# Performance work log

Measured on AMD Instinct MI355X. Metric: run time of the kernel, lower is better.

Reference implementation:

```python
import jax, jax.numpy as jnp
import numpy as np

T, B, V, D, H = 64, 256, 50000, 300, 512


def setup_inputs() -> dict:
    key = jax.random.key(0)
    ks = jax.random.split(key, 12)
    return {
        "s1": jax.random.randint(ks[0], (T, B), 0, V, dtype=jnp.int32),
        "s2": jax.random.randint(ks[1], (T, B), 0, V, dtype=jnp.int32),
        "emb_table": jax.random.normal(ks[2], (V, D), dtype=jnp.float32),
        "W_ih": jax.random.normal(ks[3], (4 * H, D), dtype=jnp.float32) * 0.2 / np.sqrt(H * D),
        "W_hh": jax.random.normal(ks[4], (4 * H, H), dtype=jnp.float32) * 0.2 / np.sqrt(H),
        "b_ih": jax.random.uniform(ks[5], (4 * H,), dtype=jnp.float32, minval=-0.5, maxval=0.5).at[H:2 * H].set(2.5),
        "b_hh": jax.random.uniform(ks[6], (4 * H,), dtype=jnp.float32, minval=-0.5, maxval=0.5).at[H:2 * H].set(2.5),
        "h0_a": 0.2 * jax.random.normal(ks[7], (B, H), dtype=jnp.float32),
        "c0_a": 0.2 * jax.random.normal(ks[8], (B, H), dtype=jnp.float32),
        "h0_b": 0.2 * jax.random.normal(ks[9], (B, H), dtype=jnp.float32),
        "c0_b": 0.2 * jax.random.normal(ks[10], (B, H), dtype=jnp.float32),
        "is_singleton": 0,
    }


def _lstm_final_hidden(xs, h0, c0, W_ih, W_hh, b_ih, b_hh):
    # xs: [T, B, D]; PyTorch gate order i, f, g, o. Returns final hidden [B, H].
    # Precompute input projections for all timesteps in one GEMM.
    x_proj = jnp.einsum("tbd,gd->tbg", xs, W_ih) + b_ih + b_hh  # [T, B, 4H]

    def step(carry, xp):
        h, c = carry
        gates = xp + h @ W_hh.T  # [B, 4H]
        i, f, g, o = jnp.split(gates, 4, axis=-1)
        c = jax.nn.sigmoid(f) * c + jax.nn.sigmoid(i) * jnp.tanh(g)
        h = jax.nn.sigmoid(o) * jnp.tanh(c)
        return (h, c), None

    (h, c), _ = jax.lax.scan(step, (h0, c0), x_proj)
    return h


def reference(s1, s2, emb_table, W_ih, W_hh, b_ih, b_hh, h0_a, c0_a, h0_b, c0_b, is_singleton):
    xa = emb_table[s1]  # [T, B, D]
    xb = emb_table[s2]
    ha = _lstm_final_hidden(xa, h0_a, c0_a, W_ih, W_hh, b_ih, b_hh)  # [B, H]
    hb = _lstm_final_hidden(xb, h0_b, c0_b, W_ih, W_hh, b_ih, b_hh)
    diff = jnp.abs(ha - hb)
    if is_singleton:
        return jnp.exp(-jnp.sum(diff))  # scalar
    return jnp.exp(-jnp.sum(diff, axis=1))  # [B]
```

## Files before the change

### kernel.cpp

```cpp
#include <hip/hip_runtime.h>
#include <hip/hip_bf16.h>
#include <math.h>

#define TT 64
#define BB 256
#define BT 512
#define DD 300
#define HH 512
#define G4 2048
#define KX 320
#define KW 512
#define KC 64
#define NCHX 5
#define NCHH 8

typedef __attribute__((ext_vector_type(8))) short short8v;
typedef __attribute__((ext_vector_type(4))) float f32x4;
typedef __attribute__((ext_vector_type(4))) unsigned short ushort4v;

__device__ __forceinline__ unsigned short f2bf(float f) {
    union { float f; unsigned int u; } v; v.f = f;
    unsigned int u = v.u;
    u += 0x7fffu + ((u >> 16) & 1u);
    return (unsigned short)(u >> 16);
}
__device__ __forceinline__ float bf2f(unsigned short s) {
    union { unsigned int u; float f; } v; v.u = ((unsigned int)s) << 16;
    return v.f;
}
__device__ __forceinline__ float sigm(float x) { return 1.0f / (1.0f + __expf(-x)); }
__device__ __forceinline__ float tanh_f(float x) {
    float ax = fabsf(x);
    if (ax > 15.0f) return (x > 0.0f) ? 1.0f : -1.0f;
    float e = __expf(2.0f * ax);
    float t = 1.0f - 2.0f / (e + 1.0f);
    return (x >= 0.0f) ? t : -t;
}

__global__ __launch_bounds__(256) void prep_w(const float* __restrict__ Wih,
                                              const float* __restrict__ Whh,
                                              const float* __restrict__ bih,
                                              const float* __restrict__ bhh,
                                              unsigned short* __restrict__ WcatP,
                                              unsigned short* __restrict__ WihP,
                                              float* __restrict__ biasP)
{
    const int gp = blockIdx.x;
    const int jt = gp >> 6, r = gp & 63;
    const int grp = r >> 4, jj = r & 15;
    const int g = grp * 512 + jt * 16 + jj;

    for (int k = threadIdx.x; k < KW; k += 256)
        WcatP[(size_t)gp * KW + k] = f2bf(Whh[(size_t)g * HH + k]);
    for (int k = threadIdx.x; k < KX; k += 256)
        WihP[(size_t)gp * KX + k] = (k < DD) ? f2bf(Wih[(size_t)g * DD + k])
                                             : (unsigned short)0;
    if (threadIdx.x == 0) biasP[jt * 64 + jj * 4 + grp] = bih[g] + bhh[g];
}

__global__ __launch_bounds__(256) void prep_h(const float* __restrict__ h0a,
                                              const float* __restrict__ c0a,
                                              const float* __restrict__ h0b,
                                              const float* __restrict__ c0b,
                                              unsigned short* __restrict__ hhi,
                                              unsigned short* __restrict__ hlo,
                                              float* __restrict__ c)
{
    const int b = blockIdx.x;
    for (int j = threadIdx.x; j < HH; j += 256) {
        float hv = (b < BB) ? h0a[b * HH + j] : h0b[(b - BB) * HH + j];
        float cv = (b < BB) ? c0a[b * HH + j] : c0b[(b - BB) * HH + j];
        unsigned short hi = f2bf(hv);
        hhi[b * HH + j] = hi;
        hlo[b * HH + j] = f2bf(hv - bf2f(hi));
        c[b * HH + j] = cv;
    }
}

__global__ __launch_bounds__(256) void gather_x(const int* __restrict__ s1,
                                                const int* __restrict__ s2,
                                                const float* __restrict__ emb,
                                                unsigned short* __restrict__ Xbf)
{
    const int idx = blockIdx.x * 256 + threadIdx.x;
    const int row = idx / 40;
    const int seg = idx - row * 40;
    const int t = row >> 9;
    const int b = row & 511;
    const int tok = (b < BB) ? s1[t * BB + b] : s2[t * BB + (b - BB)];
    const int k = seg * 8;
    short8v v;
    if (k + 8 <= DD) {
        const float* e0 = emb + (size_t)tok * DD + k;
        float4 va = *(const float4*)e0;
        float4 vb = *(const float4*)(e0 + 4);
        v[0] = (short)f2bf(va.x); v[1] = (short)f2bf(va.y);
        v[2] = (short)f2bf(va.z); v[3] = (short)f2bf(va.w);
        v[4] = (short)f2bf(vb.x); v[5] = (short)f2bf(vb.y);
        v[6] = (short)f2bf(vb.z); v[7] = (short)f2bf(vb.w);
    } else {
        #pragma unroll
        for (int e = 0; e < 8; ++e) {
            int c = k + e;
            v[e] = (c < DD) ? (short)f2bf(emb[(size_t)tok * DD + c]) : (short)0;
        }
    }
    *(short8v*)&Xbf[(size_t)row * KX + k] = v;
}

__global__ __launch_bounds__(512) void gemm_x(
    const unsigned short* __restrict__ Xbf,
    const unsigned short* __restrict__ WihP,
    unsigned short* __restrict__ xprojP)
{
    __shared__ __align__(16) unsigned short smem[16896];
    unsigned short* const As = smem;
    unsigned short* const Bs = smem + 8192;

    const int tid = threadIdx.x;
    const int xcd   = blockIdx.x & 7;
    const int local = blockIdx.x >> 3;
    const int mblk  = xcd * 32 + (local >> 4);
    const int nblk  = local & 15;

    const int lane = tid & 63;
    const int wv  = tid >> 6;
    const int wr2 = wv >> 2;
    const int wc4 = wv & 3;
    const int r16 = lane & 15;
    const int kg8 = lane >> 4;

    const int srow = tid >> 2;
    const int q2   = (tid & 3) * 2;

    f32x4 acc[4][2] = {};

    auto load_chunk = [&](int ch, short8v* va, short8v* vb) {
        const int k0 = ch * KC;
        #pragma unroll
        for (int e = 0; e < 2; ++e) {
            va[e] = *(const short8v*)(Xbf + (size_t)(mblk * 128 + srow) * KX + k0 + (q2 + e) * 8);
            vb[e] = *(const short8v*)(WihP + (size_t)(nblk * 128 + srow) * KX + k0 + (q2 + e) * 8);
        }
    };
    auto write_chunk = [&](const short8v* va, const short8v* vb) {
        #pragma unroll
        for (int e = 0; e < 2; ++e) {
            const int g = ((q2 + e) ^ (srow & 7)) << 3;
            *(short8v*)&As[srow * 64 + g] = va[e];
            *(short8v*)&Bs[srow * 64 + g] = vb[e];
        }
    };
    auto lidx = [&](int r, int ko) { return r * 64 + ((((ko) >> 3) ^ (r & 7)) << 3); };

    short8v va[2], vb[2], na[2], nb[2];
    load_chunk(0, va, vb);
    for (int ch = 0; ch < NCHX; ++ch) {
        write_chunk(va, vb);
        if (ch + 1 < NCHX) load_chunk(ch + 1, na, nb);
        __syncthreads();
        #pragma unroll
        for (int ks = 0; ks < KC; ks += 32) {
            const int ko = ks + kg8 * 8;
            short8v a[4], b[2];
            #pragma unroll
            for (int i = 0; i < 4; ++i)
                a[i] = *(const short8v*)&As[lidx(64 * wr2 + 16 * i + r16, ko)];
            #pragma unroll
            for (int j = 0; j < 2; ++j)
                b[j] = *(const short8v*)&Bs[lidx(32 * wc4 + 16 * j + r16, ko)];
            #pragma unroll
            for (int i = 0; i < 4; ++i)
                #pragma unroll
                for (int j = 0; j < 2; ++j)
                    acc[i][j] = __builtin_amdgcn_mfma_f32_16x16x32_bf16(a[i], b[j], acc[i][j], 0, 0, 0);
        }
        __syncthreads();
        #pragma unroll
        for (int e = 0; e < 2; ++e) { va[e] = na[e]; vb[e] = nb[e]; }
    }

    float* gbuf = (float*)smem;
    const int jj5 = tid & 31;
    const int hh  = jj5 >> 4;
    const int jj  = jj5 & 15;
    const int row0 = tid >> 5;
    #pragma unroll
    for (int p = 0; p < 2; ++p) {
        if (p) __syncthreads();
        if (wr2 == p) {
            #pragma unroll
            for (int i = 0; i < 4; ++i)
                #pragma unroll
                for (int j = 0; j < 2; ++j)
                    #pragma unroll
                    for (int r = 0; r < 4; ++r)
                        gbuf[(16 * i + 4 * kg8 + r) * 132 + 32 * wc4 + 16 * j + r16]
                            = acc[i][j][r];
        }
        __syncthreads();
        #pragma unroll
        for (int u = 0; u < 4; ++u) {
            const int row = row0 + 16 * u;
            const size_t m = (size_t)(mblk * 128 + p * 64 + row);
            ushort4v o;
            #pragma unroll
            for (int grp = 0; grp < 4; ++grp)
                o[grp] = f2bf(gbuf[row * 132 + hh * 64 + grp * 16 + jj]);
            __builtin_nontemporal_store(o,
                (ushort4v*)&xprojP[m * G4 + (nblk * 2 + hh) * 64 + jj * 4]);
        }
    }
}

__global__ __launch_bounds__(256) void lstm_step(
    const unsigned short* __restrict__ WcatP,
    const float* __restrict__ biasP,
    const unsigned short* __restrict__ xprojP,
    const unsigned short* __restrict__ hhi_in,
    const unsigned short* __restrict__ hlo_in,
    float* __restrict__ cbuf,
    unsigned short* __restrict__ hhi_out,
    unsigned short* __restrict__ hlo_out,
    int t)
{
    __shared__ __align__(16) unsigned short As0[64 * 64], As1[64 * 64];
    __shared__ __align__(16) unsigned short Bs0[64 * 64], Bs1[64 * 64];
    __shared__ __align__(16) float gbuf[64 * 65];

    const int tid = threadIdx.x;
    const int bid = blockIdx.x;

    const int xcd   = bid & 7;
    const int local = bid >> 3;
    const int bx    = local & 7;
    const int jt    = xcd * 4 + (local >> 3);

    const int lane = tid & 63;
    const int w = tid >> 6;
    const int wr = w >> 1, wc = w & 1;
    const int r16 = lane & 15;
    const int kg8 = lane >> 4;
    const int sl8 = lane >> 3;
    const int gd  = lane & 7;

    f32x4 acc[2][2] = {};

    auto load_chunk = [&](int ch, short8v* va, short8v* vb) {
        const int k0 = ch * KC;
        const unsigned short* abase = hhi_in + (size_t)(bx * 64) * HH + k0;
        #pragma unroll
        for (int s = 0; s < 2; ++s) {
            const int r = w * 16 + s * 8 + sl8;
            va[s] = *(const short8v*)(abase + (size_t)r * HH + gd * 8);
            vb[s] = *(const short8v*)(WcatP + (size_t)(jt * 64 + r) * KW + k0 + gd * 8);
        }
    };
    auto write_chunk = [&](unsigned short* A, unsigned short* B,
                           const short8v* va, const short8v* vb) {
        #pragma unroll
        for (int s = 0; s < 2; ++s) {
            const int r = w * 16 + s * 8 + sl8;
            const int g = (gd ^ sl8) << 3;
            *(short8v*)&A[r * 64 + g] = va[s];
            *(short8v*)&B[r * 64 + g] = vb[s];
        }
    };
    auto lidx = [&](int r, int ko) { return r * 64 + ((((ko) >> 3) ^ (r & 7)) << 3); };
    auto compute = [&](const unsigned short* A, const unsigned short* B) {
        #pragma unroll
        for (int ks = 0; ks < KC; ks += 32) {
            const int ko = ks + kg8 * 8;
            short8v a0 = *(const short8v*)&A[lidx(32 * wr + r16,      ko)];
            short8v a1 = *(const short8v*)&A[lidx(32 * wr + 16 + r16, ko)];
            short8v b0 = *(const short8v*)&B[lidx(32 * wc + r16,      ko)];
            short8v b1 = *(const short8v*)&B[lidx(32 * wc + 16 + r16, ko)];
            acc[0][0] = __builtin_amdgcn_mfma_f32_16x16x32_bf16(a0, b0, acc[0][0], 0, 0, 0);
            acc[0][1] = __builtin_amdgcn_mfma_f32_16x16x32_bf16(a0, b1, acc[0][1], 0, 0, 0);
            acc[1][0] = __builtin_amdgcn_mfma_f32_16x16x32_bf16(a1, b0, acc[1][0], 0, 0, 0);
            acc[1][1] = __builtin_amdgcn_mfma_f32_16x16x32_bf16(a1, b1, acc[1][1], 0, 0, 0);
        }
    };

    short8v ra[2], rb[2], sa[2], sb[2];
    load_chunk(0, ra, rb);
    load_chunk(1, sa, sb);

    const int jj = tid & 15;
    const int row0 = tid >> 4;
    const f32x4 bp = *(const f32x4*)&biasP[jt * 64 + jj * 4];
    ushort4v xp[4]; float cp[4];
    #pragma unroll
    for (int u = 0; u < 4; ++u) {
        int batch = bx * 64 + row0 + 16 * u;
        xp[u] = __builtin_nontemporal_load(
            (const ushort4v*)&xprojP[((size_t)t * BT + batch) * G4 + jt * 64 + jj * 4]);
        cp[u] = cbuf[batch * HH + jt * 16 + jj];
    }

    write_chunk(As0, Bs0, ra, rb);
    __syncthreads();

    for (int ch = 0; ch < NCHH; ch += 2) {
        if (ch + 2 < NCHH) load_chunk(ch + 2, ra, rb);
        write_chunk(As1, Bs1, sa, sb);
        compute(As0, Bs0);
        __syncthreads();
        if (ch + 3 < NCHH) load_chunk(ch + 3, sa, sb);
        if (ch + 2 < NCHH) write_chunk(As0, Bs0, ra, rb);
        compute(As1, Bs1);
        __syncthreads();
    }

    #pragma unroll
    for (int i = 0; i < 2; ++i)
        #pragma unroll
        for (int j2 = 0; j2 < 2; ++j2)
            #pragma unroll
            for (int r = 0; r < 4; ++r) {
                int grow = (2 * wr + i) * 16 + kg8 * 4 + r;
                int gcol = (2 * wc + j2) * 16 + r16;
                gbuf[grow * 65 + gcol] = acc[i][j2][r];
            }
    __syncthreads();

    #pragma unroll
    for (int u = 0; u < 4; ++u) {
        int row = row0 + 16 * u;
        int batch = bx * 64 + row;
        int j = jt * 16 + jj;
        float gi = gbuf[row * 65 +      jj] + bp[0] + bf2f(xp[u][0]);
        float gf = gbuf[row * 65 + 16 + jj] + bp[1] + bf2f(xp[u][1]);
        float gg = gbuf[row * 65 + 32 + jj] + bp[2] + bf2f(xp[u][2]);
        float go = gbuf[row * 65 + 48 + jj] + bp[3] + bf2f(xp[u][3]);
        float cn = sigm(gf) * cp[u] + sigm(gi) * tanh_f(gg);
        float hn = sigm(go) * tanh_f(cn);
        cbuf[batch * HH + j] = cn;
        unsigned short hi = f2bf(hn);
        hhi_out[batch * HH + j] = hi;
        hlo_out[batch * HH + j] = f2bf(hn - bf2f(hi));
    }
}

__global__ __launch_bounds__(64) void finalize(const unsigned short* __restrict__ hhi,
                                               const unsigned short* __restrict__ hlo,
                                               float* __restrict__ out)
{
    const int b = blockIdx.x;
    const int lane = threadIdx.x;
    float s = 0.0f;
    for (int j = lane; j < HH; j += 64) {
        float ha = bf2f(hhi[b * HH + j]) + bf2f(hlo[b * HH + j]);
        float hb = bf2f(hhi[(b + BB) * HH + j]) + bf2f(hlo[(b + BB) * HH + j]);
        s += fabsf(ha - hb);
    }
    #pragma unroll
    for (int off = 32; off > 0; off >>= 1) s += __shfl_down(s, off);
    if (lane == 0) out[b] = expf(-s);
}

extern "C" void kernel_launch(void* const* d_in, const int* in_sizes, int n_in,
                              void* d_out, int out_size, void* d_ws, size_t ws_size,
                              hipStream_t stream)
{
    const int*   s1  = (const int*)d_in[0];
    const int*   s2  = (const int*)d_in[1];
    const float* emb = (const float*)d_in[2];
    const float* Wih = (const float*)d_in[3];
    const float* Whh = (const float*)d_in[4];
    const float* bih = (const float*)d_in[5];
    const float* bhh = (const float*)d_in[6];
    const float* h0a = (const float*)d_in[7];
    const float* c0a = (const float*)d_in[8];
    const float* h0b = (const float*)d_in[9];
    const float* c0b = (const float*)d_in[10];
    float* out = (float*)d_out;

    char* ws = (char*)d_ws;
    size_t off = 0;
    unsigned short* WcatP = (unsigned short*)(ws + off); off += (size_t)G4 * KW * 2;
    unsigned short* WihP  = (unsigned short*)(ws + off); off += (size_t)G4 * KX * 2;
    float* biasP          = (float*)(ws + off);          off += (size_t)G4 * 4;
    unsigned short* hhi0  = (unsigned short*)(ws + off); off += (size_t)BT * HH * 2;
    unsigned short* hhi1  = (unsigned short*)(ws + off); off += (size_t)BT * HH * 2;
    unsigned short* hlo0  = (unsigned short*)(ws + off); off += (size_t)BT * HH * 2;
    unsigned short* hlo1  = (unsigned short*)(ws + off); off += (size_t)BT * HH * 2;
    float* cbuf           = (float*)(ws + off);          off += (size_t)BT * HH * 4;
    unsigned short* Xbf   = (unsigned short*)(ws + off); off += (size_t)TT * BT * KX * 2;
    unsigned short* xprojP= (unsigned short*)(ws + off); off += (size_t)TT * BT * G4 * 2;

    prep_w<<<G4, 256, 0, stream>>>(Wih, Whh, bih, bhh, WcatP, WihP, biasP);
    prep_h<<<BT, 256, 0, stream>>>(h0a, c0a, h0b, c0b, hhi0, hlo0, cbuf);
    gather_x<<<(TT * BT * 40) / 256, 256, 0, stream>>>(s1, s2, emb, Xbf);
    gemm_x<<<4096, 512, 0, stream>>>(Xbf, WihP, xprojP);

    unsigned short* hhi[2] = { hhi0, hhi1 };
    unsigned short* hlo[2] = { hlo0, hlo1 };
    for (int t = 0; t < TT; ++t) {
        int pi = t & 1, po = pi ^ 1;
        lstm_step<<<256, 256, 0, stream>>>(WcatP, biasP, xprojP,
                                           hhi[pi], hlo[pi], cbuf,
                                           hhi[po], hlo[po], t);
    }
    finalize<<<BB, 64, 0, stream>>>(hhi0, hlo0, out);
}
```

Before: 464.6 us.

## Load full W_hh tile to LDS once and read h directly from global

The per-step LSTM kernel drops the double-buffered 64-wide K-chunk pipeline. It now stages the whole 64x512 weight tile into swizzled LDS up front and streams the hidden-state A operand straight from global memory into registers for the MFMA loop. The LDS buffer is reused afterwards for the gate scratch buffer, and launch bounds now request two blocks per SIMD. This cuts the number of barriers in the K loop and the LDS round-trip for A. The trade-offs are a larger LDS footprint per block, which can limit occupancy, and uncoalesced global loads for A.

Result: slower. 837.6 us (+80.3%).

```diff
diff --git a/kernel.cpp b/kernel.cpp
--- a/kernel.cpp
+++ b/kernel.cpp
@@ -12,11 +12,12 @@
 #define KW 512
 #define KC 64
 #define NCHX 5
-#define NCHH 8
 
 typedef __attribute__((ext_vector_type(8))) short short8v;
 typedef __attribute__((ext_vector_type(4))) float f32x4;
 typedef __attribute__((ext_vector_type(4))) unsigned short ushort4v;
+
+#define MF(a, b, c) __builtin_amdgcn_mfma_f32_16x16x32_bf16(a, b, c, 0, 0, 0)
 
 __device__ __forceinline__ unsigned short f2bf(float f) {
     union { float f; unsigned int u; } v; v.f = f;
@@ -213,7 +214,7 @@
     }
 }
 
-__global__ __launch_bounds__(256) void lstm_step(
+__global__ __launch_bounds__(256, 2) void lstm_step(
     const unsigned short* __restrict__ WcatP,
     const float* __restrict__ biasP,
     const unsigned short* __restrict__ xprojP,
@@ -224,9 +225,7 @@
     unsigned short* __restrict__ hlo_out,
     int t)
 {
-    __shared__ __align__(16) unsigned short As0[64 * 64], As1[64 * 64];
-    __shared__ __align__(16) unsigned short Bs0[64 * 64], Bs1[64 * 64];
-    __shared__ __align__(16) float gbuf[64 * 65];
+    __shared__ __align__(16) unsigned short Bsm[64 * 512];
 
     const int tid = threadIdx.x;
     const int bid = blockIdx.x;
@@ -241,50 +240,18 @@
     const int wr = w >> 1, wc = w & 1;
     const int r16 = lane & 15;
     const int kg8 = lane >> 4;
-    const int sl8 = lane >> 3;
-    const int gd  = lane & 7;
-
-    f32x4 acc[2][2] = {};
-
-    auto load_chunk = [&](int ch, short8v* va, short8v* vb) {
-        const int k0 = ch * KC;
-        const unsigned short* abase = hhi_in + (size_t)(bx * 64) * HH + k0;
-        #pragma unroll
-        for (int s = 0; s < 2; ++s) {
-            const int r = w * 16 + s * 8 + sl8;
-            va[s] = *(const short8v*)(abase + (size_t)r * HH + gd * 8);
-            vb[s] = *(const short8v*)(WcatP + (size_t)(jt * 64 + r) * KW + k0 + gd * 8);
-        }
-    };
-    auto write_chunk = [&](unsigned short* A, unsigned short* B,
-                           const short8v* va, const short8v* vb) {
-        #pragma unroll
-        for (int s = 0; s < 2; ++s) {
-            const int r = w * 16 + s * 8 + sl8;
-            const int g = (gd ^ sl8) << 3;
-            *(short8v*)&A[r * 64 + g] = va[s];
-            *(short8v*)&B[r * 64 + g] = vb[s];
-        }
-    };
-    auto lidx = [&](int r, int ko) { return r * 64 + ((((ko) >> 3) ^ (r & 7)) << 3); };
-    auto compute = [&](const unsigned short* A, const unsigned short* B) {
-        #pragma unroll
-        for (int ks = 0; ks < KC; ks += 32) {
-            const int ko = ks + kg8 * 8;
-            short8v a0 = *(const short8v*)&A[lidx(32 * wr + r16,      ko)];
-            short8v a1 = *(const short8v*)&A[lidx(32 * wr + 16 + r16, ko)];
-            short8v b0 = *(const short8v*)&B[lidx(32 * wc + r16,      ko)];
-            short8v b1 = *(const short8v*)&B[lidx(32 * wc + 16 + r16, ko)];
-            acc[0][0] = __builtin_amdgcn_mfma_f32_16x16x32_bf16(a0, b0, acc[0][0], 0, 0, 0);
-            acc[0][1] = __builtin_amdgcn_mfma_f32_16x16x32_bf16(a0, b1, acc[0][1], 0, 0, 0);
-            acc[1][0] = __builtin_amdgcn_mfma_f32_16x16x32_bf16(a1, b0, acc[1][0], 0, 0, 0);
-            acc[1][1] = __builtin_amdgcn_mfma_f32_16x16x32_bf16(a1, b1, acc[1][1], 0, 0, 0);
-        }
-    };
-
-    short8v ra[2], rb[2], sa[2], sb[2];
-    load_chunk(0, ra, rb);
-    load_chunk(1, sa, sb);
+
+    {
+        const int r  = tid >> 2;
+        const int q0 = (tid & 3) * 16;
+        const unsigned short* bsrc = WcatP + (size_t)(jt * 64 + r) * KW;
+        #pragma unroll
+        for (int i = 0; i < 16; ++i) {
+            const int q  = q0 + i;
+            const int qs = q ^ (r & 7);
+            *(short8v*)&Bsm[r * 512 + qs * 8] = *(const short8v*)(bsrc + q * 8);
+        }
+    }
 
     const int jj = tid & 15;
     const int row0 = tid >> 4;
@@ -298,20 +265,31 @@
         cp[u] = cbuf[batch * HH + jt * 16 + jj];
     }
 
-    write_chunk(As0, Bs0, ra, rb);
     __syncthreads();
 
-    for (int ch = 0; ch < NCHH; ch += 2) {
-        if (ch + 2 < NCHH) load_chunk(ch + 2, ra, rb);
-        write_chunk(As1, Bs1, sa, sb);
-        compute(As0, Bs0);
-        __syncthreads();
-        if (ch + 3 < NCHH) load_chunk(ch + 3, sa, sb);
-        if (ch + 2 < NCHH) write_chunk(As0, Bs0, ra, rb);
-        compute(As1, Bs1);
-        __syncthreads();
-    }
-
+    const unsigned short* arow0 = hhi_in + (size_t)(bx * 64 + 32 * wr + r16) * HH;
+    const unsigned short* arow1 = arow0 + (size_t)16 * HH;
+    const int br0 = (32 * wc + r16) * 512;
+    const int br1 = br0 + 16 * 512;
+
+    f32x4 acc[2][2] = {};
+    #pragma unroll
+    for (int ks = 0; ks < 16; ++ks) {
+        const int ko = ks * 32 + kg8 * 8;
+        const int qs = ((ks * 4 + kg8) ^ (r16 & 7)) * 8;
+        short8v a0 = *(const short8v*)(arow0 + ko);
+        short8v a1 = *(const short8v*)(arow1 + ko);
+        short8v b0 = *(const short8v*)&Bsm[br0 + qs];
+        short8v b1 = *(const short8v*)&Bsm[br1 + qs];
+        acc[0][0] = MF(a0, b0, acc[0][0]);
+        acc[0][1] = MF(a0, b1, acc[0][1]);
+        acc[1][0] = MF(a1, b0, acc[1][0]);
+        acc[1][1] = MF(a1, b1, acc[1][1]);
+    }
+
+    __syncthreads();
+
+    float* gbuf = (float*)Bsm;
     #pragma unroll
     for (int i = 0; i < 2; ++i)
         #pragma unroll
```
